# Kernel optimization log

Hardware: AMD Instinct MI355X
Metric: run time of the kernel (lower is better)

The kernel has to match this reference:

```python
import jax, jax.numpy as jnp
import numpy as np

N, D, E, EDGE_DIM = 50000, 128, 800000, 3
NEG_SLOPE = 0.2
LN_EPS = 1e-5


def setup_inputs() -> dict:
    key = jax.random.key(0)
    ks = jax.random.split(key, 12)
    s = 1.0 / np.sqrt(D)
    return {
        "x": jax.random.normal(ks[0], (N, D), jnp.float32),
        "edge_index": jax.random.randint(ks[1], (2, E), 0, N, jnp.int32),
        "edge_attr": jax.random.normal(ks[2], (E, EDGE_DIM), jnp.float32),
        "W_l": jax.random.normal(ks[3], (D, D), jnp.float32) * s,
        "b_l": jnp.zeros((D,), jnp.float32),
        "W_r": jax.random.normal(ks[4], (D, D), jnp.float32) * s,
        "b_r": jnp.zeros((D,), jnp.float32),
        "W_e": jax.random.normal(ks[5], (EDGE_DIM, D), jnp.float32) * (1.0 / np.sqrt(EDGE_DIM)),
        "att": jax.random.normal(ks[6], (D,), jnp.float32) * s,
        "bias": jnp.zeros((D,), jnp.float32),
        "res_weight": jnp.array(0.1, jnp.float32),
        "ln_gamma": jnp.ones((D,), jnp.float32),
        "ln_beta": jnp.zeros((D,), jnp.float32),
    }


def reference(x, edge_index, edge_attr, W_l, b_l, W_r, b_r, W_e, att, bias,
              res_weight, ln_gamma, ln_beta):
    src, dst = edge_index[0], edge_index[1]
    # GATv2: lin_l on source, lin_r on target (heads=1, concat=False)
    x_l = x @ W_l + b_l            # [N, D]
    x_r = x @ W_r + b_r            # [N, D]
    e_emb = edge_attr @ W_e        # [E, D]
    # per-edge attention logits
    m = x_l[src] + x_r[dst] + e_emb                      # [E, D]
    m = jnp.where(m > 0, m, NEG_SLOPE * m)               # leaky_relu(0.2)
    alpha = m @ att                                       # [E]
    # segment softmax over destination nodes
    seg_max = jax.ops.segment_max(alpha, dst, num_segments=N)
    seg_max = jnp.where(jnp.isfinite(seg_max), seg_max, 0.0)
    ex = jnp.exp(alpha - seg_max[dst])
    seg_sum = jax.ops.segment_sum(ex, dst, num_segments=N)
    alpha = ex / (seg_sum[dst] + 1e-16)                   # [E]
    # weighted aggregation of transformed source features (dropout off / eval)
    msgs = x_l[src] * alpha[:, None]                      # [E, D]
    out = jax.ops.segment_sum(msgs, dst, num_segments=N) + bias  # [N, D]
    # residual + LayerNorm
    out = x + res_weight * out
    mu = jnp.mean(out, axis=-1, keepdims=True)
    var = jnp.mean(jnp.square(out - mu), axis=-1, keepdims=True)
    out = (out - mu) * jax.lax.rsqrt(var + LN_EPS)
    return out * ln_gamma + ln_beta
```

## Files before the change

kernel.cpp:

```cpp
#include <hip/hip_runtime.h>
#include <hip/hip_bf16.h>

#define N_NODES 50000
#define DIM 128
#define N_EDGES 800000
#define NEG_SLOPE 0.2f
#define LN_EPS 1e-5f
#define SCAN_BS 256
#define NB_SCAN ((N_NODES + SCAN_BS - 1) / SCAN_BS)
#define PADCAP (N_EDGES + 4 * N_NODES)


__global__ __launch_bounds__(256) void lin_kernel(
    const float* __restrict__ x,
    const float* __restrict__ Wl, const float* __restrict__ bl,
    const float* __restrict__ Wr, const float* __restrict__ br,
    __hip_bfloat16* __restrict__ xl_bf, float* __restrict__ xr)
{
    __shared__ float xs[8][DIM];
    const int node0 = blockIdx.x * 8;
    const int t = threadIdx.x;
    for (int i = t; i < 8 * DIM; i += 256) {
        int n = node0 + (i >> 7);
        xs[i >> 7][i & 127] = (n < N_NODES) ? x[(size_t)n * DIM + (i & 127)] : 0.f;
    }
    __syncthreads();
    const int d = t & 127;
    const bool is_l = (t < 128);
    const float* W = is_l ? Wl : Wr;
    const float* b = is_l ? bl : br;
    float acc[8];
#pragma unroll
    for (int i = 0; i < 8; i++) acc[i] = b[d];
    for (int k = 0; k < DIM; k++) {
        float w = W[k * DIM + d];
#pragma unroll
        for (int i = 0; i < 8; i++) acc[i] += xs[i][k] * w;
    }
#pragma unroll
    for (int i = 0; i < 8; i++) {
        int n = node0 + i;
        if (n < N_NODES) {
            if (is_l) xl_bf[(size_t)n * DIM + d] = __float2bfloat16(acc[i]);
            else      xr[(size_t)n * DIM + d] = acc[i];
        }
    }
}

__global__ __launch_bounds__(256) void hist_kernel(const int* __restrict__ dst_idx,
                                                   int* __restrict__ cnt) {
    int e = blockIdx.x * 256 + threadIdx.x;
    if (e < N_EDGES) atomicAdd(&cnt[dst_idx[e]], 1);
}

__global__ __launch_bounds__(SCAN_BS) void scan1_kernel(int* __restrict__ cnt,
                                                        int* __restrict__ partials) {
    __shared__ int sh[SCAN_BS];
    const int i = blockIdx.x * SCAN_BS + threadIdx.x;
    const int deg = (i < N_NODES) ? cnt[i] : 0;
    const int v = (deg + 3) & ~3;
    sh[threadIdx.x] = v;
    __syncthreads();
    for (int off = 1; off < SCAN_BS; off <<= 1) {
        int u = (threadIdx.x >= off) ? sh[threadIdx.x - off] : 0;
        __syncthreads();
        sh[threadIdx.x] += u;
        __syncthreads();
    }
    if (i < N_NODES) cnt[i] = sh[threadIdx.x] - v;
    if (threadIdx.x == SCAN_BS - 1) partials[blockIdx.x] = sh[threadIdx.x];
}

__global__ __launch_bounds__(SCAN_BS) void scan2_kernel(int* __restrict__ partials) {
    __shared__ int sh[SCAN_BS];
    const int t = threadIdx.x;
    const int v = (t < NB_SCAN) ? partials[t] : 0;
    sh[t] = v;
    __syncthreads();
    for (int off = 1; off < SCAN_BS; off <<= 1) {
        int u = (t >= off) ? sh[t - off] : 0;
        __syncthreads();
        sh[t] += u;
        __syncthreads();
    }
    if (t < NB_SCAN) partials[t] = sh[t] - v;
}

__global__ __launch_bounds__(SCAN_BS) void scan3_kernel(int* __restrict__ cnt,
                                                        const int* __restrict__ partials,
                                                        int* __restrict__ cursor) {
    const int i = blockIdx.x * SCAN_BS + threadIdx.x;
    if (i < N_NODES) {
        int rs = cnt[i] + partials[blockIdx.x];
        cnt[i] = rs;
        cursor[i] = rs;
    }
}

__global__ __launch_bounds__(256) void scatter_kernel(
    const int* __restrict__ src_idx, const int* __restrict__ dst_idx,
    const float* __restrict__ ea,
    int* __restrict__ cursor,
    int* __restrict__ sorted_src, float* __restrict__ sorted_ea) {
    int e = blockIdx.x * 256 + threadIdx.x;
    if (e >= N_EDGES) return;
    int pos = atomicAdd(&cursor[dst_idx[e]], 1);
    sorted_src[pos] = src_idx[e];
    sorted_ea[3 * pos + 0] = ea[(size_t)e * 3 + 0];
    sorted_ea[3 * pos + 1] = ea[(size_t)e * 3 + 1];
    sorted_ea[3 * pos + 2] = ea[(size_t)e * 3 + 2];
}

__global__ __launch_bounds__(256) void fused_node_kernel(
    const float* __restrict__ x, const __hip_bfloat16* __restrict__ xl_bf,
    const int* __restrict__ row_start, const int* __restrict__ cursor,
    const int* __restrict__ sorted_src, const float* __restrict__ sorted_ea,
    const float* __restrict__ We, const float* __restrict__ att,
    const float* __restrict__ bias, const float* __restrict__ rw_p,
    const float* __restrict__ gamma, const float* __restrict__ beta,
    float* __restrict__ out)
{
    const int v = blockIdx.x * 4 + (threadIdx.x >> 6);
    const int lane = threadIdx.x & 63;
    if (v >= N_NODES) return;
    const int begin = row_start[v];
    const int end   = cursor[v];
    const size_t nb = (size_t)v * DIM + 2 * lane;
    const float2 xrv = *(const float2*)&out[nb];
    const float2 at  = *(const float2*)&att[2 * lane];
    const float2 we0 = *(const float2*)&We[0 * DIM + 2 * lane];
    const float2 we1 = *(const float2*)&We[1 * DIM + 2 * lane];
    const float2 we2 = *(const float2*)&We[2 * DIM + 2 * lane];

    float m = -3.4e38f, s = 0.f, a0 = 0.f, a1 = 0.f;
    int pos = begin;

    for (; pos + 4 <= end; pos += 4) {
        const int4 s4 = *(const int4*)(sorted_src + pos);
        const float4* eap = (const float4*)(sorted_ea + 3 * pos);
        const float4 eA = eap[0], eB = eap[1], eC = eap[2];
        const unsigned xu0 = *(const unsigned*)&xl_bf[(size_t)s4.x * DIM + 2 * lane];
        const unsigned xu1 = *(const unsigned*)&xl_bf[(size_t)s4.y * DIM + 2 * lane];
        const unsigned xu2 = *(const unsigned*)&xl_bf[(size_t)s4.z * DIM + 2 * lane];
        const unsigned xu3 = *(const unsigned*)&xl_bf[(size_t)s4.w * DIM + 2 * lane];
        const float xl00 = __uint_as_float(xu0 << 16), xl10 = __uint_as_float(xu0 & 0xffff0000u);
        const float xl01 = __uint_as_float(xu1 << 16), xl11 = __uint_as_float(xu1 & 0xffff0000u);
        const float xl02 = __uint_as_float(xu2 << 16), xl12 = __uint_as_float(xu2 & 0xffff0000u);
        const float xl03 = __uint_as_float(xu3 << 16), xl13 = __uint_as_float(xu3 & 0xffff0000u);

        float P0, P1, P2, P3;
        {
            float t0, t1;
            t0 = xl00 + xrv.x + eA.x * we0.x + eA.y * we1.x + eA.z * we2.x;
            t1 = xl10 + xrv.y + eA.x * we0.y + eA.y * we1.y + eA.z * we2.y;
            t0 = t0 > 0.f ? t0 : NEG_SLOPE * t0;  t1 = t1 > 0.f ? t1 : NEG_SLOPE * t1;
            P0 = t0 * at.x + t1 * at.y;
            t0 = xl01 + xrv.x + eA.w * we0.x + eB.x * we1.x + eB.y * we2.x;
            t1 = xl11 + xrv.y + eA.w * we0.y + eB.x * we1.y + eB.y * we2.y;
            t0 = t0 > 0.f ? t0 : NEG_SLOPE * t0;  t1 = t1 > 0.f ? t1 : NEG_SLOPE * t1;
            P1 = t0 * at.x + t1 * at.y;
            t0 = xl02 + xrv.x + eB.z * we0.x + eB.w * we1.x + eC.x * we2.x;
            t1 = xl12 + xrv.y + eB.z * we0.y + eB.w * we1.y + eC.x * we2.y;
            t0 = t0 > 0.f ? t0 : NEG_SLOPE * t0;  t1 = t1 > 0.f ? t1 : NEG_SLOPE * t1;
            P2 = t0 * at.x + t1 * at.y;
            t0 = xl03 + xrv.x + eC.y * we0.x + eC.z * we1.x + eC.w * we2.x;
            t1 = xl13 + xrv.y + eC.y * we0.y + eC.z * we1.y + eC.w * we2.y;
            t0 = t0 > 0.f ? t0 : NEG_SLOPE * t0;  t1 = t1 > 0.f ? t1 : NEG_SLOPE * t1;
            P3 = t0 * at.x + t1 * at.y;
        }
        const float tA0 = __shfl_xor(P0, 1, 64);
        const float tA1 = __shfl_xor(P1, 1, 64);
        const float tB0 = __shfl_xor(P2, 1, 64);
        const float tB1 = __shfl_xor(P3, 1, 64);
        const bool b0 = (lane & 1);
        float A = b0 ? (P1 + tA1) : (P0 + tA0);
        float B = b0 ? (P3 + tB1) : (P2 + tB0);
        const float tA = __shfl_xor(A, 2, 64);
        const float tB = __shfl_xor(B, 2, 64);
        float C = (lane & 2) ? (B + tB) : (A + tA);
        C += __shfl_xor(C, 4, 64);
        C += __shfl_xor(C, 8, 64);
        C += __shfl_xor(C, 16, 64);
        C += __shfl_xor(C, 32, 64);
        const int base = lane & ~3;
        const float p0 = __shfl(C, base + 0, 64);
        const float p1 = __shfl(C, base + 1, 64);
        const float p2 = __shfl(C, base + 2, 64);
        const float p3 = __shfl(C, base + 3, 64);

        const float pm = fmaxf(fmaxf(p0, p1), fmaxf(p2, p3));
        if (pm <= m + 8.f) {
            const float w0 = __expf(p0 - m), w1 = __expf(p1 - m);
            const float w2 = __expf(p2 - m), w3 = __expf(p3 - m);
            s  += (w0 + w1) + (w2 + w3);
            a0 += w0 * xl00 + w1 * xl01 + w2 * xl02 + w3 * xl03;
            a1 += w0 * xl10 + w1 * xl11 + w2 * xl12 + w3 * xl13;
        } else {
            const float mn = fmaxf(m, pm);
            const float f  = __expf(m - mn);
            const float w0 = __expf(p0 - mn), w1 = __expf(p1 - mn);
            const float w2 = __expf(p2 - mn), w3 = __expf(p3 - mn);
            s  = s  * f + (w0 + w1) + (w2 + w3);
            a0 = a0 * f + w0 * xl00 + w1 * xl01 + w2 * xl02 + w3 * xl03;
            a1 = a1 * f + w0 * xl10 + w1 * xl11 + w2 * xl12 + w3 * xl13;
            m = mn;
        }
    }

    for (; pos < end; ++pos) {
        const int sn = sorted_src[pos];
        const float ea0 = sorted_ea[3 * pos + 0];
        const float ea1 = sorted_ea[3 * pos + 1];
        const float ea2 = sorted_ea[3 * pos + 2];
        const unsigned xu = *(const unsigned*)&xl_bf[(size_t)sn * DIM + 2 * lane];
        const float xl0 = __uint_as_float(xu << 16);
        const float xl1 = __uint_as_float(xu & 0xffff0000u);
        float t0 = xl0 + xrv.x + ea0 * we0.x + ea1 * we1.x + ea2 * we2.x;
        float t1 = xl1 + xrv.y + ea0 * we0.y + ea1 * we1.y + ea2 * we2.y;
        t0 = t0 > 0.f ? t0 : NEG_SLOPE * t0;
        t1 = t1 > 0.f ? t1 : NEG_SLOPE * t1;
        float p = t0 * at.x + t1 * at.y;
#pragma unroll
        for (int o = 32; o > 0; o >>= 1) p += __shfl_xor(p, o, 64);
        if (p <= m + 8.f) {
            const float w = __expf(p - m);
            s += w; a0 += w * xl0; a1 += w * xl1;
        } else {
            const float mn = fmaxf(m, p);
            const float f = __expf(m - mn);
            const float w = __expf(p - mn);
            s = s * f + w; a0 = a0 * f + w * xl0; a1 = a1 * f + w * xl1;
            m = mn;
        }
    }

    const float inv = 1.f / (s + 1e-16f);

    const float2 xv = *(const float2*)&x[nb];
    const float rw = rw_p[0];
    float v0 = xv.x + rw * (a0 * inv + bias[2 * lane]);
    float v1 = xv.y + rw * (a1 * inv + bias[2 * lane + 1]);
    float sum = v0 + v1;
#pragma unroll
    for (int o = 32; o > 0; o >>= 1) sum += __shfl_xor(sum, o, 64);
    const float mu = sum * (1.f / DIM);
    const float d0 = v0 - mu, d1 = v1 - mu;
    float q = d0 * d0 + d1 * d1;
#pragma unroll
    for (int o = 32; o > 0; o >>= 1) q += __shfl_xor(q, o, 64);
    const float rstd = rsqrtf(q * (1.f / DIM) + LN_EPS);
    float2 r;
    r.x = d0 * rstd * gamma[2 * lane]     + beta[2 * lane];
    r.y = d1 * rstd * gamma[2 * lane + 1] + beta[2 * lane + 1];
    *(float2*)&out[nb] = r;
}

extern "C" void kernel_launch(void* const* d_in, const int* in_sizes, int n_in,
                              void* d_out, int out_size, void* d_ws, size_t ws_size,
                              hipStream_t stream)
{
    const float* x    = (const float*)d_in[0];
    const int*   ei   = (const int*)d_in[1];
    const float* ea   = (const float*)d_in[2];
    const float* Wl   = (const float*)d_in[3];
    const float* bl   = (const float*)d_in[4];
    const float* Wr   = (const float*)d_in[5];
    const float* br   = (const float*)d_in[6];
    const float* We   = (const float*)d_in[7];
    const float* att  = (const float*)d_in[8];
    const float* bias = (const float*)d_in[9];
    const float* rw   = (const float*)d_in[10];
    const float* gmm  = (const float*)d_in[11];
    const float* bta  = (const float*)d_in[12];
    float* out = (float*)d_out;

    const int* src_idx = ei;
    const int* dst_idx = ei + N_EDGES;

    __hip_bfloat16* xl_bf = (__hip_bfloat16*)d_ws;
    int*   sorted_src = (int*)(xl_bf + (size_t)N_NODES * DIM);
    float* sorted_ea  = (float*)(sorted_src + PADCAP);
    int*   row_start  = (int*)(sorted_ea + (size_t)3 * PADCAP);
    int*   cursor     = row_start + N_NODES;
    int*   partials   = cursor + N_NODES;

    hipMemsetAsync(row_start, 0, (size_t)N_NODES * sizeof(int), stream);
    hist_kernel<<<(N_EDGES + 255) / 256, 256, 0, stream>>>(dst_idx, row_start);
    scan1_kernel<<<NB_SCAN, SCAN_BS, 0, stream>>>(row_start, partials);
    scan2_kernel<<<1, SCAN_BS, 0, stream>>>(partials);
    scan3_kernel<<<NB_SCAN, SCAN_BS, 0, stream>>>(row_start, partials, cursor);
    scatter_kernel<<<(N_EDGES + 255) / 256, 256, 0, stream>>>(src_idx, dst_idx, ea,
                                                              cursor, sorted_src, sorted_ea);
    lin_kernel<<<(N_NODES + 7) / 8, 256, 0, stream>>>(x, Wl, bl, Wr, br, xl_bf, out);
    fused_node_kernel<<<(N_NODES + 3) / 4, 256, 0, stream>>>(x, xl_bf, row_start, cursor,
                                                             sorted_src, sorted_ea,
                                                             We, att, bias, rw, gmm, bta, out);
}
```

Before: 348.7 us.

## Pack edge records as float4, software-pipeline gathers, vectorize histogram

Each sorted edge's three attributes and its source index are now stored together as one float4, so the scatter does a single 16-byte write and the node kernel a single vector read per edge. The node kernel's 4-edge loop now prefetches the next group's packed records and bf16 feature gathers while the current group is being computed, to hide gather latency. The histogram reads destination indices four at a time, and the lin kernel's k-loop gets an unroll hint. The prefetching adds register pressure, which could lower occupancy.

```diff
diff --git a/kernel.cpp b/kernel.cpp
--- a/kernel.cpp
+++ b/kernel.cpp
@@ -32,6 +32,7 @@
     float acc[8];
 #pragma unroll
     for (int i = 0; i < 8; i++) acc[i] = b[d];
+#pragma unroll 4
     for (int k = 0; k < DIM; k++) {
         float w = W[k * DIM + d];
 #pragma unroll
@@ -49,8 +50,17 @@
 
 __global__ __launch_bounds__(256) void hist_kernel(const int* __restrict__ dst_idx,
                                                    int* __restrict__ cnt) {
-    int e = blockIdx.x * 256 + threadIdx.x;
-    if (e < N_EDGES) atomicAdd(&cnt[dst_idx[e]], 1);
+    int i = blockIdx.x * 256 + threadIdx.x;
+    int e = i * 4;
+    if (e + 4 <= N_EDGES) {
+        const int4 d4 = *(const int4*)(dst_idx + e);
+        atomicAdd(&cnt[d4.x], 1);
+        atomicAdd(&cnt[d4.y], 1);
+        atomicAdd(&cnt[d4.z], 1);
+        atomicAdd(&cnt[d4.w], 1);
+    } else {
+        for (; e < N_EDGES; ++e) atomicAdd(&cnt[dst_idx[e]], 1);
+    }
 }
 
 __global__ __launch_bounds__(SCAN_BS) void scan1_kernel(int* __restrict__ cnt,
@@ -100,21 +110,22 @@
 __global__ __launch_bounds__(256) void scatter_kernel(
     const int* __restrict__ src_idx, const int* __restrict__ dst_idx,
     const float* __restrict__ ea,
-    int* __restrict__ cursor,
-    int* __restrict__ sorted_src, float* __restrict__ sorted_ea) {
+    int* __restrict__ cursor, float4* __restrict__ packed) {
     int e = blockIdx.x * 256 + threadIdx.x;
     if (e >= N_EDGES) return;
     int pos = atomicAdd(&cursor[dst_idx[e]], 1);
-    sorted_src[pos] = src_idx[e];
-    sorted_ea[3 * pos + 0] = ea[(size_t)e * 3 + 0];
-    sorted_ea[3 * pos + 1] = ea[(size_t)e * 3 + 1];
-    sorted_ea[3 * pos + 2] = ea[(size_t)e * 3 + 2];
+    float4 p;
+    p.x = ea[(size_t)e * 3 + 0];
+    p.y = ea[(size_t)e * 3 + 1];
+    p.z = ea[(size_t)e * 3 + 2];
+    p.w = __int_as_float(src_idx[e]);
+    packed[pos] = p;
 }
 
 __global__ __launch_bounds__(256) void fused_node_kernel(
     const float* __restrict__ x, const __hip_bfloat16* __restrict__ xl_bf,
     const int* __restrict__ row_start, const int* __restrict__ cursor,
-    const int* __restrict__ sorted_src, const float* __restrict__ sorted_ea,
+    const float4* __restrict__ packed,
     const float* __restrict__ We, const float* __restrict__ att,
     const float* __restrict__ bias, const float* __restrict__ rw_p,
     const float* __restrict__ gamma, const float* __restrict__ beta,
@@ -126,23 +137,36 @@
     const int begin = row_start[v];
     const int end   = cursor[v];
     const size_t nb = (size_t)v * DIM + 2 * lane;
+    const int loff = 2 * lane;
     const float2 xrv = *(const float2*)&out[nb];
-    const float2 at  = *(const float2*)&att[2 * lane];
-    const float2 we0 = *(const float2*)&We[0 * DIM + 2 * lane];
-    const float2 we1 = *(const float2*)&We[1 * DIM + 2 * lane];
-    const float2 we2 = *(const float2*)&We[2 * DIM + 2 * lane];
+    const float2 at  = *(const float2*)&att[loff];
+    const float2 we0 = *(const float2*)&We[0 * DIM + loff];
+    const float2 we1 = *(const float2*)&We[1 * DIM + loff];
+    const float2 we2 = *(const float2*)&We[2 * DIM + loff];
 
     float m = -3.4e38f, s = 0.f, a0 = 0.f, a1 = 0.f;
     int pos = begin;
-
-    for (; pos + 4 <= end; pos += 4) {
-        const int4 s4 = *(const int4*)(sorted_src + pos);
-        const float4* eap = (const float4*)(sorted_ea + 3 * pos);
-        const float4 eA = eap[0], eB = eap[1], eC = eap[2];
-        const unsigned xu0 = *(const unsigned*)&xl_bf[(size_t)s4.x * DIM + 2 * lane];
-        const unsigned xu1 = *(const unsigned*)&xl_bf[(size_t)s4.y * DIM + 2 * lane];
-        const unsigned xu2 = *(const unsigned*)&xl_bf[(size_t)s4.z * DIM + 2 * lane];
-        const unsigned xu3 = *(const unsigned*)&xl_bf[(size_t)s4.w * DIM + 2 * lane];
+    const int full_end = begin + ((end - begin) & ~3);
+
+    float4 pk0, pk1, pk2, pk3;
+    unsigned xu0, xu1, xu2, xu3;
+    if (pos < full_end) {
+        pk0 = packed[pos];     pk1 = packed[pos + 1];
+        pk2 = packed[pos + 2]; pk3 = packed[pos + 3];
+        xu0 = *(const unsigned*)&xl_bf[(size_t)__float_as_int(pk0.w) * DIM + loff];
+        xu1 = *(const unsigned*)&xl_bf[(size_t)__float_as_int(pk1.w) * DIM + loff];
+        xu2 = *(const unsigned*)&xl_bf[(size_t)__float_as_int(pk2.w) * DIM + loff];
+        xu3 = *(const unsigned*)&xl_bf[(size_t)__float_as_int(pk3.w) * DIM + loff];
+    }
+
+    while (pos < full_end) {
+        const int npos = pos + 4;
+        const bool more = npos < full_end;
+        float4 nk0, nk1, nk2, nk3;
+        if (more) {
+            nk0 = packed[npos];     nk1 = packed[npos + 1];
+            nk2 = packed[npos + 2]; nk3 = packed[npos + 3];
+        }
         const float xl00 = __uint_as_float(xu0 << 16), xl10 = __uint_as_float(xu0 & 0xffff0000u);
         const float xl01 = __uint_as_float(xu1 << 16), xl11 = __uint_as_float(xu1 & 0xffff0000u);
         const float xl02 = __uint_as_float(xu2 << 16), xl12 = __uint_as_float(xu2 & 0xffff0000u);
@@ -151,22 +175,29 @@
         float P0, P1, P2, P3;
         {
             float t0, t1;
-            t0 = xl00 + xrv.x + eA.x * we0.x + eA.y * we1.x + eA.z * we2.x;
-            t1 = xl10 + xrv.y + eA.x * we0.y + eA.y * we1.y + eA.z * we2.y;
+            t0 = xl00 + xrv.x + pk0.x * we0.x + pk0.y * we1.x + pk0.z * we2.x;
+            t1 = xl10 + xrv.y + pk0.x * we0.y + pk0.y * we1.y + pk0.z * we2.y;
             t0 = t0 > 0.f ? t0 : NEG_SLOPE * t0;  t1 = t1 > 0.f ? t1 : NEG_SLOPE * t1;
             P0 = t0 * at.x + t1 * at.y;
-            t0 = xl01 + xrv.x + eA.w * we0.x + eB.x * we1.x + eB.y * we2.x;
-            t1 = xl11 + xrv.y + eA.w * we0.y + eB.x * we1.y + eB.y * we2.y;
+            t0 = xl01 + xrv.x + pk1.x * we0.x + pk1.y * we1.x + pk1.z * we2.x;
+            t1 = xl11 + xrv.y + pk1.x * we0.y + pk1.y * we1.y + pk1.z * we2.y;
             t0 = t0 > 0.f ? t0 : NEG_SLOPE * t0;  t1 = t1 > 0.f ? t1 : NEG_SLOPE * t1;
             P1 = t0 * at.x + t1 * at.y;
-            t0 = xl02 + xrv.x + eB.z * we0.x + eB.w * we1.x + eC.x * we2.x;
-            t1 = xl12 + xrv.y + eB.z * we0.y + eB.w * we1.y + eC.x * we2.y;
+            t0 = xl02 + xrv.x + pk2.x * we0.x + pk2.y * we1.x + pk2.z * we2.x;
+            t1 = xl12 + xrv.y + pk2.x * we0.y + pk2.y * we1.y + pk2.z * we2.y;
             t0 = t0 > 0.f ? t0 : NEG_SLOPE * t0;  t1 = t1 > 0.f ? t1 : NEG_SLOPE * t1;
             P2 = t0 * at.x + t1 * at.y;
-            t0 = xl03 + xrv.x + eC.y * we0.x + eC.z * we1.x + eC.w * we2.x;
-            t1 = xl13 + xrv.y + eC.y * we0.y + eC.z * we1.y + eC.w * we2.y;
+            t0 = xl03 + xrv.x + pk3.x * we0.x + pk3.y * we1.x + pk3.z * we2.x;
+            t1 = xl13 + xrv.y + pk3.x * we0.y + pk3.y * we1.y + pk3.z * we2.y;
             t0 = t0 > 0.f ? t0 : NEG_SLOPE * t0;  t1 = t1 > 0.f ? t1 : NEG_SLOPE * t1;
             P3 = t0 * at.x + t1 * at.y;
+        }
+        unsigned nu0, nu1, nu2, nu3;
+        if (more) {
+            nu0 = *(const unsigned*)&xl_bf[(size_t)__float_as_int(nk0.w) * DIM + loff];
+            nu1 = *(const unsigned*)&xl_bf[(size_t)__float_as_int(nk1.w) * DIM + loff];
+            nu2 = *(const unsigned*)&xl_bf[(size_t)__float_as_int(nk2.w) * DIM + loff];
+            nu3 = *(const unsigned*)&xl_bf[(size_t)__float_as_int(nk3.w) * DIM + loff];
         }
         const float tA0 = __shfl_xor(P0, 1, 64);
         const float tA1 = __shfl_xor(P1, 1, 64);
@@ -205,18 +236,19 @@
             a1 = a1 * f + w0 * xl10 + w1 * xl11 + w2 * xl12 + w3 * xl13;
             m = mn;
         }
+        pk0 = nk0; pk1 = nk1; pk2 = nk2; pk3 = nk3;
+        xu0 = nu0; xu1 = nu1; xu2 = nu2; xu3 = nu3;
+        pos = npos;
     }
 
     for (; pos < end; ++pos) {
-        const int sn = sorted_src[pos];
-        const float ea0 = sorted_ea[3 * pos + 0];
-        const float ea1 = sorted_ea[3 * pos + 1];
-        const float ea2 = sorted_ea[3 * pos + 2];
-        const unsigned xu = *(const unsigned*)&xl_bf[(size_t)sn * DIM + 2 * lane];
+        const float4 pk = packed[pos];
+        const int sn = __float_as_int(pk.w);
+        const unsigned xu = *(const unsigned*)&xl_bf[(size_t)sn * DIM + loff];
         const float xl0 = __uint_as_float(xu << 16);
         const float xl1 = __uint_as_float(xu & 0xffff0000u);
-        float t0 = xl0 + xrv.x + ea0 * we0.x + ea1 * we1.x + ea2 * we2.x;
-        float t1 = xl1 + xrv.y + ea0 * we0.y + ea1 * we1.y + ea2 * we2.y;
+        float t0 = xl0 + xrv.x + pk.x * we0.x + pk.y * we1.x + pk.z * we2.x;
+        float t1 = xl1 + xrv.y + pk.x * we0.y + pk.y * we1.y + pk.z * we2.y;
         t0 = t0 > 0.f ? t0 : NEG_SLOPE * t0;
         t1 = t1 > 0.f ? t1 : NEG_SLOPE * t1;
         float p = t0 * at.x + t1 * at.y;
@@ -238,8 +270,8 @@
 
     const float2 xv = *(const float2*)&x[nb];
     const float rw = rw_p[0];
-    float v0 = xv.x + rw * (a0 * inv + bias[2 * lane]);
-    float v1 = xv.y + rw * (a1 * inv + bias[2 * lane + 1]);
+    float v0 = xv.x + rw * (a0 * inv + bias[loff]);
+    float v1 = xv.y + rw * (a1 * inv + bias[loff + 1]);
     float sum = v0 + v1;
 #pragma unroll
     for (int o = 32; o > 0; o >>= 1) sum += __shfl_xor(sum, o, 64);
@@ -250,8 +282,8 @@
     for (int o = 32; o > 0; o >>= 1) q += __shfl_xor(q, o, 64);
     const float rstd = rsqrtf(q * (1.f / DIM) + LN_EPS);
     float2 r;
-    r.x = d0 * rstd * gamma[2 * lane]     + beta[2 * lane];
-    r.y = d1 * rstd * gamma[2 * lane + 1] + beta[2 * lane + 1];
+    r.x = d0 * rstd * gamma[loff]     + beta[loff];
+    r.y = d1 * rstd * gamma[loff + 1] + beta[loff + 1];
     *(float2*)&out[nb] = r;
 }
 
@@ -278,21 +310,20 @@
     const int* dst_idx = ei + N_EDGES;
 
     __hip_bfloat16* xl_bf = (__hip_bfloat16*)d_ws;
-    int*   sorted_src = (int*)(xl_bf + (size_t)N_NODES * DIM);
-    float* sorted_ea  = (float*)(sorted_src + PADCAP);
-    int*   row_start  = (int*)(sorted_ea + (size_t)3 * PADCAP);
+    float4* packed    = (float4*)(xl_bf + (size_t)N_NODES * DIM);
+    int*   row_start  = (int*)(packed + PADCAP);
     int*   cursor     = row_start + N_NODES;
     int*   partials   = cursor + N_NODES;
 
     hipMemsetAsync(row_start, 0, (size_t)N_NODES * sizeof(int), stream);
-    hist_kernel<<<(N_EDGES + 255) / 256, 256, 0, stream>>>(dst_idx, row_start);
+    hist_kernel<<<(N_EDGES / 4 + 255) / 256, 256, 0, stream>>>(dst_idx, row_start);
     scan1_kernel<<<NB_SCAN, SCAN_BS, 0, stream>>>(row_start, partials);
     scan2_kernel<<<1, SCAN_BS, 0, stream>>>(partials);
     scan3_kernel<<<NB_SCAN, SCAN_BS, 0, stream>>>(row_start, partials, cursor);
     scatter_kernel<<<(N_EDGES + 255) / 256, 256, 0, stream>>>(src_idx, dst_idx, ea,
-                                                              cursor, sorted_src, sorted_ea);
+                                                              cursor, packed);
     lin_kernel<<<(N_NODES + 7) / 8, 256, 0, stream>>>(x, Wl, bl, Wr, br, xl_bf, out);
     fused_node_kernel<<<(N_NODES + 3) / 4, 256, 0, stream>>>(x, xl_bf, row_start, cursor,
-                                                             sorted_src, sorted_ea,
+                                                             packed,
                                                              We, att, bias, rw, gmm, bta, out);
 }
```

Measured after the change: 366.2 us. 1.05x slower.
